# Kernel optimization log

Measured on AMD Instinct MI355X. Metric: run time of the kernel, lower is better.

Reference implementation:

```python
import jax, jax.numpy as jnp
import numpy as np

N, L, D_MODEL, N_HEADS = 2, 2048, 512, 8

def setup_inputs() -> dict:
    key = jax.random.key(0)
    x = jax.random.normal(key, (N, L, D_MODEL), dtype=jnp.float32)
    return {"input_data": x}

def reference(input_data):
    n, l, _ = input_data.shape
    h = N_HEADS
    d = D_MODEL // h  # head dim
    # Q = K = V = reshaped input (the Linear projections are unused in the original forward)
    q = input_data.reshape(n, l, h, d)
    k = q
    v = q
    scale = 1.0 / jnp.sqrt(jnp.float32(d))
    # scores: [n, h, l, s]
    scores = jnp.einsum('nlhd,nshd->nhls', q, k)
    attn_weights = jax.nn.softmax(scale * scores, axis=-1)
    # updated values: [n, l, h, d]
    updated_v = jnp.einsum('nhls,nshd->nlhd', attn_weights, v)
    out = updated_v.reshape(n, l, h * d)
    # attn returned as mean over heads: permute nhls -> nlhs, mean over h -> [n, l, s]
    attn = jnp.transpose(attn_weights, (0, 2, 1, 3)).mean(axis=-2)
    return (out, attn)
```

## Files before the change

kernel.cpp:

```cpp
#include <hip/hip_runtime.h>

#define NBATCH 2
#define SEQ    2048
#define DMODEL 512
#define NH     8
#define HDIM   64
#define SCALE  0.125f

#define K2 0.1803368801111204f

#if __has_builtin(__builtin_amdgcn_exp2f)
#define EXP2(x) __builtin_amdgcn_exp2f(x)
#else
#define EXP2(x) __expf((x) * 0.6931471805599453f)
#endif

typedef __attribute__((ext_vector_type(8))) short bf16x8;
typedef __attribute__((ext_vector_type(4))) float f32x4;

__device__ __forceinline__ unsigned short f2bf(float f) {
    union { float f; unsigned u; } v; v.f = f;
    unsigned r = v.u + 0x7FFFu + ((v.u >> 16) & 1u);
    return (unsigned short)(r >> 16);
}

__device__ __forceinline__ void pack4(unsigned short* dst, float4 v) {
    unsigned long long pk = (unsigned long long)f2bf(v.x)
        | ((unsigned long long)f2bf(v.y) << 16)
        | ((unsigned long long)f2bf(v.z) << 32)
        | ((unsigned long long)f2bf(v.w) << 48);
    __builtin_memcpy(dst, &pk, 8);
}

__device__ __forceinline__ bf16x8 pack8(float4 a, float4 b) {
    bf16x8 r;
    r[0]=(short)f2bf(a.x); r[1]=(short)f2bf(a.y); r[2]=(short)f2bf(a.z); r[3]=(short)f2bf(a.w);
    r[4]=(short)f2bf(b.x); r[5]=(short)f2bf(b.y); r[6]=(short)f2bf(b.z); r[7]=(short)f2bf(b.w);
    return r;
}

__device__ __forceinline__ void gld_lds16(const unsigned short* g, unsigned short* l) {
    __builtin_amdgcn_global_load_lds(
        (const __attribute__((address_space(1))) unsigned int*)(const void*)g,
        (__attribute__((address_space(3))) unsigned int*)(void*)l, 16, 0, 0);
}

__global__ __launch_bounds__(256) void prep_kernel(const float* __restrict__ x,
                                                   unsigned short* __restrict__ xb,
                                                   unsigned short* __restrict__ xt) {
    __shared__ unsigned short Tb[64][72];
    const int bid = blockIdx.x;
    const int n = bid >> 8, h = (bid >> 5) & 7, st = bid & 31;
    const int s0 = st * 64;
    const int t = threadIdx.x;
    {
        const int s = t >> 2, d0 = (t & 3) * 16;
        const float* xp = x + ((size_t)(n*SEQ + s0 + s))*DMODEL + h*HDIM + d0;
        #pragma unroll
        for (int i = 0; i < 4; ++i) pack4(&Tb[s][d0 + 4*i], *(const float4*)(xp + 4*i));
    }
    __syncthreads();
    {
        const int s = t >> 2, d0 = (t & 3) * 16;
        unsigned short* bp = xb + ((size_t)(n*SEQ + s0 + s))*DMODEL + h*HDIM + d0;
        *(bf16x8*)bp       = *(const bf16x8*)&Tb[s][d0];
        *(bf16x8*)(bp + 8) = *(const bf16x8*)&Tb[s][d0 + 8];
    }
    {
        const int d = t >> 2, c0 = (t & 3) * 16;
        bf16x8 v0, v1;
        #pragma unroll
        for (int j = 0; j < 8; ++j) {
            v0[j] = (short)Tb[c0 + j][d];
            v1[j] = (short)Tb[c0 + 8 + j][d];
        }
        unsigned short* tp = xt + ((size_t)((n*NH + h)*HDIM + d))*SEQ + s0 + c0;
        *(bf16x8*)tp       = v0;
        *(bf16x8*)(tp + 8) = v1;
    }
}

__global__ __launch_bounds__(256) void out_kernel4(const unsigned short* __restrict__ xb,
                                                   const unsigned short* __restrict__ xt,
                                                   float* __restrict__ out,
                                                   float* __restrict__ rho,
                                                   float* __restrict__ part,
                                                   int split) {
    __shared__ unsigned short Kb[2][64*64];
    __shared__ unsigned short Vt[2][64*64];
    __shared__ unsigned short pb[64][72];

    const int i   = blockIdx.x;
    const int cps = gridDim.x >> 3;
    const int bid = (i & 7) * cps + (i >> 3);
    int n, h, lt, ss;
    if (split) { n = bid >> 9; h = (bid >> 6) & 7; lt = (bid >> 1) & 31; ss = bid & 1; }
    else       { n = bid >> 8; h = (bid >> 5) & 7; lt = bid & 31;        ss = 0;       }
    const int l0 = lt * 64;
    const int sbase = ss << 10;
    const int nch = split ? 16 : 32;

    const int tid = threadIdx.x;
    const int wv = tid >> 6, lane = tid & 63;
    const int lr = lane & 15, lg = lane >> 4;

    const unsigned short* qp = xb + ((size_t)(n*SEQ + l0 + wv*16 + lr))*DMODEL + h*HDIM + lg*8;
    const bf16x8 a0 = *(const bf16x8*)qp;
    const bf16x8 a1 = *(const bf16x8*)(qp + 32);

    bf16x8 ones;
    #pragma unroll
    for (int j = 0; j < 8; ++j) ones[j] = (short)0x3F80;

    const int srow8  = wv*8 + (lane >> 3);
    const int schunk = lane & 7;
    const unsigned short* kbase = xb + (size_t)(n*SEQ)*DMODEL + h*HDIM;
    const unsigned short* vbase = xt + ((size_t)(n*NH + h)*HDIM)*SEQ;

    auto stage = [&](int buf, int s0) {
        #pragma unroll
        for (int it = 0; it < 2; ++it) {
            const int row = it*32 + srow8;
            const int gc  = schunk ^ (row & 7);
            gld_lds16(kbase + (size_t)(s0 + row)*DMODEL + gc*8,
                      &Kb[buf][it*2048 + wv*512]);
        }
        #pragma unroll
        for (int it = 0; it < 2; ++it) {
            const int d  = it*32 + srow8;
            const int gc = schunk ^ (d & 7);
            gld_lds16(vbase + (size_t)d*SEQ + s0 + gc*8,
                      &Vt[buf][it*2048 + wv*512]);
        }
    };

    f32x4 ov0 = {0.f,0.f,0.f,0.f}, ov1 = {0.f,0.f,0.f,0.f};
    f32x4 ov2 = {0.f,0.f,0.f,0.f}, ov3 = {0.f,0.f,0.f,0.f};
    f32x4 ovS = {0.f,0.f,0.f,0.f};

    stage(0, sbase);
    __syncthreads();
    int cur = 0;

    for (int c = 0; c < nch; ++c) {
        if (c < nch - 1) stage(cur ^ 1, sbase + (c + 1) * 64);

        const int c0 = (lg ^ (lr & 7)) << 3;
        #pragma unroll
        for (int ct = 0; ct < 4; ++ct) {
            const unsigned short* kr = &Kb[cur][(ct*16 + lr)*64];
            bf16x8 b0 = *(const bf16x8*)&kr[c0];
            bf16x8 b1 = *(const bf16x8*)&kr[c0 ^ 32];
            f32x4 acc = {0.f,0.f,0.f,0.f};
            acc = __builtin_amdgcn_mfma_f32_16x16x32_bf16(b0, a0, acc, 0,0,0);
            acc = __builtin_amdgcn_mfma_f32_16x16x32_bf16(b1, a1, acc, 0,0,0);
            const float e0 = EXP2(acc[0] * K2);
            const float e1 = EXP2(acc[1] * K2);
            const float e2 = EXP2(acc[2] * K2);
            const float e3 = EXP2(acc[3] * K2);
            unsigned long long pk = (unsigned long long)f2bf(e0)
                | ((unsigned long long)f2bf(e1) << 16)
                | ((unsigned long long)f2bf(e2) << 32)
                | ((unsigned long long)f2bf(e3) << 48);
            __builtin_memcpy(&pb[wv*16 + lr][ct*16 + lg*4], &pk, 8);
        }
        #pragma unroll
        for (int ks = 0; ks < 2; ++ks) {
            const bf16x8 pa = *(const bf16x8*)&pb[wv*16 + lr][ks*32 + lg*8];
            const int cc = ((ks*4 + lg) ^ (lr & 7)) << 3;
            const bf16x8 w0 = *(const bf16x8*)&Vt[cur][( 0 + lr)*64 + cc];
            const bf16x8 w1 = *(const bf16x8*)&Vt[cur][(16 + lr)*64 + cc];
            const bf16x8 w2 = *(const bf16x8*)&Vt[cur][(32 + lr)*64 + cc];
            const bf16x8 w3 = *(const bf16x8*)&Vt[cur][(48 + lr)*64 + cc];
            ov0 = __builtin_amdgcn_mfma_f32_16x16x32_bf16(pa, w0, ov0, 0,0,0);
            ov1 = __builtin_amdgcn_mfma_f32_16x16x32_bf16(pa, w1, ov1, 0,0,0);
            ov2 = __builtin_amdgcn_mfma_f32_16x16x32_bf16(pa, w2, ov2, 0,0,0);
            ov3 = __builtin_amdgcn_mfma_f32_16x16x32_bf16(pa, w3, ov3, 0,0,0);
            ovS = __builtin_amdgcn_mfma_f32_16x16x32_bf16(pa, ones, ovS, 0,0,0);
        }
        __syncthreads();
        cur ^= 1;
    }

    if (split) {
        float* pp = part + ((size_t)(((n*NH + h)*32 + lt)*2 + ss))*4160;
        #pragma unroll
        for (int r = 0; r < 4; ++r) {
            const int qloc = wv*16 + lg*4 + r;
            float* op = pp + qloc*64 + lr;
            op[0]  = ov0[r];
            op[16] = ov1[r];
            op[32] = ov2[r];
            op[48] = ov3[r];
        }
        if (lr == 0) {
            #pragma unroll
            for (int r = 0; r < 4; ++r)
                pp[4096 + wv*16 + lg*4 + r] = ovS[r];
        }
    } else {
        const int row0 = l0 + wv*16 + lg*4;
        if (lr == 0) {
            #pragma unroll
            for (int r = 0; r < 4; ++r)
                rho[(size_t)(n*NH + h)*SEQ + row0 + r] = ovS[r];
        }
        #pragma unroll
        for (int r = 0; r < 4; ++r) {
            const float iv = 1.f / ovS[r];
            float* op = out + ((size_t)(n*SEQ + row0 + r))*DMODEL + h*HDIM + lr;
            op[0]  = ov0[r] * iv;
            op[16] = ov1[r] * iv;
            op[32] = ov2[r] * iv;
            op[48] = ov3[r] * iv;
        }
    }
}

__global__ __launch_bounds__(256) void combine_kernel(const float* __restrict__ part,
                                                      float* __restrict__ out,
                                                      float* __restrict__ rho) {
    const int bid = blockIdx.x;
    const int n = bid >> 8, h = (bid >> 5) & 7, lt = bid & 31;
    const int l0 = lt * 64;
    const int tid = threadIdx.x;
    const int q = tid >> 2, dg = (tid & 3) * 16;

    const float* p0 = part + ((size_t)(((n*NH + h)*32 + lt)*2))*4160;
    const float* p1 = p0 + 4160;
    const float rs = p0[4096 + q] + p1[4096 + q];
    const float iv = 1.f / rs;
    if ((tid & 3) == 0)
        rho[(size_t)(n*NH + h)*SEQ + l0 + q] = rs;

    float* op = out + ((size_t)(n*SEQ + l0 + q))*DMODEL + h*HDIM + dg;
    #pragma unroll
    for (int i = 0; i < 4; ++i) {
        float4 a = *(const float4*)&p0[q*64 + dg + 4*i];
        float4 b = *(const float4*)&p1[q*64 + dg + 4*i];
        float4 o = { (a.x+b.x)*iv, (a.y+b.y)*iv, (a.z+b.z)*iv, (a.w+b.w)*iv };
        *(float4*)&op[4*i] = o;
    }
}

__global__ __launch_bounds__(256) void mean_kernel4(const unsigned short* __restrict__ xb,
                                                    const float* __restrict__ rho,
                                                    float* __restrict__ attn) {
    __shared__ unsigned short Qb[2][64*64];
    __shared__ unsigned short Kb[2][64*64];
    __shared__ float invb[NH][64];

    const int i   = blockIdx.x;
    const int bid = (i & 7) * 256 + (i >> 3);
    const int n = bid >> 10, lt = (bid >> 5) & 31, st = bid & 31;
    const int l0 = lt * 64, s0 = st * 64;
    const int tid = threadIdx.x;
    const int wv = tid >> 6, lane = tid & 63;
    const int lr = lane & 15, lg = lane >> 4;

    for (int j = tid; j < NH*64; j += 256) {
        const int hh = j >> 6, row = j & 63;
        invb[hh][row] = 0.125f / rho[(size_t)(n*NH + hh)*SEQ + l0 + row];
    }

    const int srow8  = wv*8 + (lane >> 3);
    const int schunk = lane & 7;

    auto stage = [&](int buf, int h) {
        #pragma unroll
        for (int it = 0; it < 2; ++it) {
            const int row = it*32 + srow8;
            const int gc  = schunk ^ (row & 7);
            gld_lds16(xb + ((size_t)(n*SEQ + l0 + row))*DMODEL + h*HDIM + gc*8,
                      &Qb[buf][it*2048 + wv*512]);
        }
        #pragma unroll
        for (int it = 0; it < 2; ++it) {
            const int row = it*32 + srow8;
            const int gc  = schunk ^ (row & 7);
            gld_lds16(xb + ((size_t)(n*SEQ + s0 + row))*DMODEL + h*HDIM + gc*8,
                      &Kb[buf][it*2048 + wv*512]);
        }
    };

    float mean[4][4];
    #pragma unroll
    for (int ct = 0; ct < 4; ++ct)
        #pragma unroll
        for (int r = 0; r < 4; ++r) mean[ct][r] = 0.f;

    stage(0, 0);
    __syncthreads();
    int cur = 0;

    for (int h = 0; h < NH; ++h) {
        if (h < NH-1) stage(cur ^ 1, h + 1);

        const int qrow = wv*16 + lr;
        const int c0 = (lg ^ (lr & 7)) << 3;
        const bf16x8 a0 = *(const bf16x8*)&Qb[cur][qrow*64 + c0];
        const bf16x8 a1 = *(const bf16x8*)&Qb[cur][qrow*64 + (c0 ^ 32)];
        const float logiv = __log2f(invb[h][wv*16 + lr]);
        #pragma unroll
        for (int ct = 0; ct < 4; ++ct) {
            const unsigned short* kr = &Kb[cur][(ct*16 + lr)*64];
            bf16x8 b0 = *(const bf16x8*)&kr[c0];
            bf16x8 b1 = *(const bf16x8*)&kr[c0 ^ 32];
            f32x4 acc = {0.f,0.f,0.f,0.f};
            acc = __builtin_amdgcn_mfma_f32_16x16x32_bf16(b0, a0, acc, 0,0,0);
            acc = __builtin_amdgcn_mfma_f32_16x16x32_bf16(b1, a1, acc, 0,0,0);
            #pragma unroll
            for (int r = 0; r < 4; ++r)
                mean[ct][r] += EXP2(fmaf(acc[r], K2, logiv));
        }
        __syncthreads();
        cur ^= 1;
    }

    const int arow = n*SEQ + l0 + wv*16 + lr;
    #pragma unroll
    for (int ct = 0; ct < 4; ++ct) {
        float4 v = { mean[ct][0], mean[ct][1], mean[ct][2], mean[ct][3] };
        *(float4*)&attn[(size_t)arow*SEQ + s0 + ct*16 + lg*4] = v;
    }
}

__global__ __launch_bounds__(256) void fb_out_kernel(const float* __restrict__ x,
                                                     float* __restrict__ out,
                                                     float* __restrict__ rho) {
    __shared__ unsigned short Kbuf[128][72];
    __shared__ unsigned short vT[64][136];
    __shared__ unsigned short pbuf[64][136];
    const int bid = blockIdx.x;
    const int n  = bid >> 8, h = (bid >> 5) & 7, lt = bid & 31;
    const int l0 = lt * 64;
    const int tid = threadIdx.x;
    const int wv  = tid >> 6, lane = tid & 63;
    const int lr  = lane & 15, lg = lane >> 4;
    const float* qp = x + ((size_t)(n*SEQ + l0 + wv*16 + lr))*DMODEL + h*HDIM + lg*8;
    const bf16x8 a0 = pack8(*(const float4*)qp,      *(const float4*)(qp+4));
    const bf16x8 a1 = pack8(*(const float4*)(qp+32), *(const float4*)(qp+36));
    f32x4 ov0 = {0.f,0.f,0.f,0.f}, ov1 = {0.f,0.f,0.f,0.f};
    f32x4 ov2 = {0.f,0.f,0.f,0.f}, ov3 = {0.f,0.f,0.f,0.f};
    float rs[4] = {0.f,0.f,0.f,0.f};
    for (int s0 = 0; s0 < SEQ; s0 += 128) {
        __syncthreads();
        {
            const int srow = tid >> 1, dbase = (tid & 1) * 32;
            const float* kp = x + ((size_t)(n*SEQ + s0 + srow))*DMODEL + h*HDIM + dbase;
            #pragma unroll
            for (int i = 0; i < 8; ++i) {
                float4 v = *(const float4*)(kp + 4*i);
                pack4(&Kbuf[srow][dbase + 4*i], v);
                const int d = dbase + 4*i;
                vT[d+0][srow] = f2bf(v.x); vT[d+1][srow] = f2bf(v.y);
                vT[d+2][srow] = f2bf(v.z); vT[d+3][srow] = f2bf(v.w);
            }
        }
        __syncthreads();
        #pragma unroll
        for (int ct = 0; ct < 8; ++ct) {
            const unsigned short* bp = &Kbuf[ct*16 + lr][lg*8];
            bf16x8 b0 = *(const bf16x8*)bp;
            bf16x8 b1 = *(const bf16x8*)(bp + 32);
            f32x4 acc = {0.f,0.f,0.f,0.f};
            acc = __builtin_amdgcn_mfma_f32_16x16x32_bf16(a0, b0, acc, 0,0,0);
            acc = __builtin_amdgcn_mfma_f32_16x16x32_bf16(a1, b1, acc, 0,0,0);
            #pragma unroll
            for (int r = 0; r < 4; ++r) {
                const float e = __expf(acc[r] * SCALE);
                rs[r] += e;
                pbuf[wv*16 + lg*4 + r][ct*16 + lr] = f2bf(e);
            }
        }
        __syncthreads();
        #pragma unroll
        for (int ks = 0; ks < 4; ++ks) {
            bf16x8 pa = *(const bf16x8*)&pbuf[wv*16 + lr][ks*32 + lg*8];
            bf16x8 v0 = *(const bf16x8*)&vT[ 0 + lr][ks*32 + lg*8];
            bf16x8 v1 = *(const bf16x8*)&vT[16 + lr][ks*32 + lg*8];
            bf16x8 v2 = *(const bf16x8*)&vT[32 + lr][ks*32 + lg*8];
            bf16x8 v3 = *(const bf16x8*)&vT[48 + lr][ks*32 + lg*8];
            ov0 = __builtin_amdgcn_mfma_f32_16x16x32_bf16(pa, v0, ov0, 0,0,0);
            ov1 = __builtin_amdgcn_mfma_f32_16x16x32_bf16(pa, v1, ov1, 0,0,0);
            ov2 = __builtin_amdgcn_mfma_f32_16x16x32_bf16(pa, v2, ov2, 0,0,0);
            ov3 = __builtin_amdgcn_mfma_f32_16x16x32_bf16(pa, v3, ov3, 0,0,0);
        }
    }
    #pragma unroll
    for (int r = 0; r < 4; ++r) {
        float s = rs[r];
        s += __shfl_xor(s, 1, 16); s += __shfl_xor(s, 2, 16);
        s += __shfl_xor(s, 4, 16); s += __shfl_xor(s, 8, 16);
        rs[r] = s;
    }
    const int row0 = l0 + wv*16 + lg*4;
    if (lr == 0) {
        #pragma unroll
        for (int r = 0; r < 4; ++r)
            rho[(size_t)(n*NH + h)*SEQ + row0 + r] = rs[r];
    }
    #pragma unroll
    for (int r = 0; r < 4; ++r) {
        const float iv = 1.f / rs[r];
        float* op = out + ((size_t)(n*SEQ + row0 + r))*DMODEL + h*HDIM + lr;
        op[0] = ov0[r]*iv; op[16] = ov1[r]*iv; op[32] = ov2[r]*iv; op[48] = ov3[r]*iv;
    }
}

__global__ __launch_bounds__(256) void fb_mean_kernel(const float* __restrict__ x,
                                                      const float* __restrict__ rho,
                                                      float* __restrict__ attn) {
    __shared__ unsigned short Qb[64][72];
    __shared__ unsigned short Kb[128][72];
    __shared__ float          invb[64];
    const int bid = blockIdx.x;
    const int n  = bid >> 9, lt = (bid >> 4) & 31, st = bid & 15;
    const int l0 = lt * 64, s0 = st * 128;
    const int tid = threadIdx.x;
    const int wv  = tid >> 6, lane = tid & 63;
    const int lr  = lane & 15, lg = lane >> 4;
    float mean[8][4];
    #pragma unroll
    for (int ct = 0; ct < 8; ++ct)
        #pragma unroll
        for (int r = 0; r < 4; ++r) mean[ct][r] = 0.f;
    for (int h = 0; h < NH; ++h) {
        __syncthreads();
        {
            const int qrow = tid >> 2, qd = (tid & 3) * 16;
            const float* qp = x + ((size_t)(n*SEQ + l0 + qrow))*DMODEL + h*HDIM + qd;
            #pragma unroll
            for (int i = 0; i < 4; ++i)
                pack4(&Qb[qrow][qd + 4*i], *(const float4*)(qp + 4*i));
        }
        {
            const int srow = tid >> 1, dbase = (tid & 1) * 32;
            const float* kp = x + ((size_t)(n*SEQ + s0 + srow))*DMODEL + h*HDIM + dbase;
            #pragma unroll
            for (int i = 0; i < 8; ++i)
                pack4(&Kb[srow][dbase + 4*i], *(const float4*)(kp + 4*i));
        }
        if (tid < 64)
            invb[tid] = 0.125f / rho[(size_t)(n*NH + h)*SEQ + l0 + tid];
        __syncthreads();
        const unsigned short* ap = &Qb[wv*16 + lr][lg*8];
        const bf16x8 a0 = *(const bf16x8*)ap;
        const bf16x8 a1 = *(const bf16x8*)(ap + 32);
        #pragma unroll
        for (int ct = 0; ct < 8; ++ct) {
            const unsigned short* bp = &Kb[ct*16 + lr][lg*8];
            bf16x8 b0 = *(const bf16x8*)bp;
            bf16x8 b1 = *(const bf16x8*)(bp + 32);
            f32x4 acc = {0.f,0.f,0.f,0.f};
            acc = __builtin_amdgcn_mfma_f32_16x16x32_bf16(a0, b0, acc, 0,0,0);
            acc = __builtin_amdgcn_mfma_f32_16x16x32_bf16(a1, b1, acc, 0,0,0);
            #pragma unroll
            for (int r = 0; r < 4; ++r)
                mean[ct][r] += __expf(acc[r] * SCALE) * invb[wv*16 + lg*4 + r];
        }
    }
    #pragma unroll
    for (int ct = 0; ct < 8; ++ct)
        #pragma unroll
        for (int r = 0; r < 4; ++r)
            attn[((size_t)(n*SEQ + l0 + wv*16 + lg*4 + r))*SEQ + s0 + ct*16 + lr]
                = mean[ct][r];
}

extern "C" void kernel_launch(void* const* d_in, const int* in_sizes, int n_in,
                              void* d_out, int out_size, void* d_ws, size_t ws_size,
                              hipStream_t stream) {
    (void)in_sizes; (void)n_in; (void)out_size;
    const float* x = (const float*)d_in[0];
    float* out  = (float*)d_out;
    float* attn = out + (size_t)NBATCH*SEQ*DMODEL;
    float* rho  = (float*)d_ws;

    const size_t XB_OFF   = 131072;
    const size_t XT_OFF   = XB_OFF + 4194304;
    const size_t NEED1    = XT_OFF + 4194304;
    const size_t PART_OFF = NEED1;
    const size_t NEED2    = PART_OFF + (size_t)1024*4160*4;

    if (ws_size >= NEED1) {
        unsigned short* xb = (unsigned short*)((char*)d_ws + XB_OFF);
        unsigned short* xt = (unsigned short*)((char*)d_ws + XT_OFF);
        prep_kernel <<<dim3(512),  dim3(256), 0, stream>>>(x, xb, xt);
        if (ws_size >= NEED2) {
            float* part = (float*)((char*)d_ws + PART_OFF);
            out_kernel4   <<<dim3(1024), dim3(256), 0, stream>>>(xb, xt, out, rho, part, 1);
            combine_kernel<<<dim3(512),  dim3(256), 0, stream>>>(part, out, rho);
        } else {
            out_kernel4   <<<dim3(512),  dim3(256), 0, stream>>>(xb, xt, out, rho, nullptr, 0);
        }
        mean_kernel4<<<dim3(2048), dim3(256), 0, stream>>>(xb, rho, attn);
    } else {
        fb_out_kernel <<<dim3(512),  dim3(256), 0, stream>>>(x, out, rho);
        fb_mean_kernel<<<dim3(1024), dim3(256), 0, stream>>>(x, rho, attn);
    }
}
```

Baseline: 84.69 us.

## Rewrite attention output kernel with 32x32x16 MFMA and register-resident P

```diff
diff --git a/kernel.cpp b/kernel.cpp
--- a/kernel.cpp
+++ b/kernel.cpp
@@ -15,8 +15,9 @@
 #define EXP2(x) __expf((x) * 0.6931471805599453f)
 #endif
 
-typedef __attribute__((ext_vector_type(8))) short bf16x8;
-typedef __attribute__((ext_vector_type(4))) float f32x4;
+typedef __attribute__((ext_vector_type(8)))  short bf16x8;
+typedef __attribute__((ext_vector_type(4)))  float f32x4;
+typedef __attribute__((ext_vector_type(16))) float f32x16;
 
 __device__ __forceinline__ unsigned short f2bf(float f) {
     union { float f; unsigned u; } v; v.f = f;
@@ -37,6 +38,12 @@
     r[0]=(short)f2bf(a.x); r[1]=(short)f2bf(a.y); r[2]=(short)f2bf(a.z); r[3]=(short)f2bf(a.w);
     r[4]=(short)f2bf(b.x); r[5]=(short)f2bf(b.y); r[6]=(short)f2bf(b.z); r[7]=(short)f2bf(b.w);
     return r;
+}
+
+__device__ __forceinline__ unsigned cvt_pk_bf16(float s0, float s1) {
+    unsigned d;
+    asm("v_cvt_pk_bf16_f32 %0, %1, %2" : "=v"(d) : "v"(s0), "v"(s1));
+    return d;
 }
 
 __device__ __forceinline__ void gld_lds16(const unsigned short* g, unsigned short* l) {
@@ -80,15 +87,14 @@
     }
 }
 
-__global__ __launch_bounds__(256) void out_kernel4(const unsigned short* __restrict__ xb,
-                                                   const unsigned short* __restrict__ xt,
-                                                   float* __restrict__ out,
-                                                   float* __restrict__ rho,
-                                                   float* __restrict__ part,
-                                                   int split) {
+__global__ __launch_bounds__(256, 4) void out_kernel5(const unsigned short* __restrict__ xb,
+                                                      const unsigned short* __restrict__ xt,
+                                                      float* __restrict__ out,
+                                                      float* __restrict__ rho,
+                                                      float* __restrict__ part,
+                                                      int split) {
     __shared__ unsigned short Kb[2][64*64];
     __shared__ unsigned short Vt[2][64*64];
-    __shared__ unsigned short pb[64][72];
 
     const int i   = blockIdx.x;
     const int cps = gridDim.x >> 3;
@@ -102,15 +108,15 @@
 
     const int tid = threadIdx.x;
     const int wv = tid >> 6, lane = tid & 63;
-    const int lr = lane & 15, lg = lane >> 4;
-
-    const unsigned short* qp = xb + ((size_t)(n*SEQ + l0 + wv*16 + lr))*DMODEL + h*HDIM + lg*8;
-    const bf16x8 a0 = *(const bf16x8*)qp;
-    const bf16x8 a1 = *(const bf16x8*)(qp + 32);
-
-    bf16x8 ones;
-    #pragma unroll
-    for (int j = 0; j < 8; ++j) ones[j] = (short)0x3F80;
+    const int lrow = lane & 31;
+    const int hi = lane >> 5;
+    const int qh = wv & 1, sh = wv >> 1;
+
+    const unsigned short* qg = xb + ((size_t)(n*SEQ + l0 + qh*32 + lrow))*DMODEL + h*HDIM;
+    bf16x8 qf[4];
+    #pragma unroll
+    for (int kst = 0; kst < 4; ++kst)
+        qf[kst] = *(const bf16x8*)(qg + kst*16 + hi*8);
 
     const int srow8  = wv*8 + (lane >> 3);
     const int schunk = lane & 7;
@@ -134,9 +140,10 @@
         }
     };
 
-    f32x4 ov0 = {0.f,0.f,0.f,0.f}, ov1 = {0.f,0.f,0.f,0.f};
-    f32x4 ov2 = {0.f,0.f,0.f,0.f}, ov3 = {0.f,0.f,0.f,0.f};
-    f32x4 ovS = {0.f,0.f,0.f,0.f};
+    f32x16 ovA = {0.f}, ovB = {0.f};
+    #pragma unroll
+    for (int r = 0; r < 16; ++r) { ovA[r] = 0.f; ovB[r] = 0.f; }
+    float rs = 0.f;
 
     stage(0, sbase);
     __syncthreads();
@@ -145,74 +152,90 @@
     for (int c = 0; c < nch; ++c) {
         if (c < nch - 1) stage(cur ^ 1, sbase + (c + 1) * 64);
 
-        const int c0 = (lg ^ (lr & 7)) << 3;
-        #pragma unroll
-        for (int ct = 0; ct < 4; ++ct) {
-            const unsigned short* kr = &Kb[cur][(ct*16 + lr)*64];
-            bf16x8 b0 = *(const bf16x8*)&kr[c0];
-            bf16x8 b1 = *(const bf16x8*)&kr[c0 ^ 32];
-            f32x4 acc = {0.f,0.f,0.f,0.f};
-            acc = __builtin_amdgcn_mfma_f32_16x16x32_bf16(b0, a0, acc, 0,0,0);
-            acc = __builtin_amdgcn_mfma_f32_16x16x32_bf16(b1, a1, acc, 0,0,0);
-            const float e0 = EXP2(acc[0] * K2);
-            const float e1 = EXP2(acc[1] * K2);
-            const float e2 = EXP2(acc[2] * K2);
-            const float e3 = EXP2(acc[3] * K2);
-            unsigned long long pk = (unsigned long long)f2bf(e0)
-                | ((unsigned long long)f2bf(e1) << 16)
-                | ((unsigned long long)f2bf(e2) << 32)
-                | ((unsigned long long)f2bf(e3) << 48);
-            __builtin_memcpy(&pb[wv*16 + lr][ct*16 + lg*4], &pk, 8);
-        }
-        #pragma unroll
-        for (int ks = 0; ks < 2; ++ks) {
-            const bf16x8 pa = *(const bf16x8*)&pb[wv*16 + lr][ks*32 + lg*8];
-            const int cc = ((ks*4 + lg) ^ (lr & 7)) << 3;
-            const bf16x8 w0 = *(const bf16x8*)&Vt[cur][( 0 + lr)*64 + cc];
-            const bf16x8 w1 = *(const bf16x8*)&Vt[cur][(16 + lr)*64 + cc];
-            const bf16x8 w2 = *(const bf16x8*)&Vt[cur][(32 + lr)*64 + cc];
-            const bf16x8 w3 = *(const bf16x8*)&Vt[cur][(48 + lr)*64 + cc];
-            ov0 = __builtin_amdgcn_mfma_f32_16x16x32_bf16(pa, w0, ov0, 0,0,0);
-            ov1 = __builtin_amdgcn_mfma_f32_16x16x32_bf16(pa, w1, ov1, 0,0,0);
-            ov2 = __builtin_amdgcn_mfma_f32_16x16x32_bf16(pa, w2, ov2, 0,0,0);
-            ov3 = __builtin_amdgcn_mfma_f32_16x16x32_bf16(pa, w3, ov3, 0,0,0);
-            ovS = __builtin_amdgcn_mfma_f32_16x16x32_bf16(pa, ones, ovS, 0,0,0);
+        f32x16 acc;
+        #pragma unroll
+        for (int r = 0; r < 16; ++r) acc[r] = 0.f;
+        #pragma unroll
+        for (int kst = 0; kst < 4; ++kst) {
+            const int g = ((kst*2 + hi) ^ (lrow & 7)) << 3;
+            const bf16x8 kf = *(const bf16x8*)&Kb[cur][(sh*32 + lrow)*64 + g];
+            acc = __builtin_amdgcn_mfma_f32_32x32x16_bf16(kf, qf[kst], acc, 0, 0, 0);
+        }
+        #pragma unroll
+        for (int r = 0; r < 16; ++r) {
+            acc[r] = EXP2(acc[r] * K2);
+            rs += acc[r];
+        }
+        #pragma unroll
+        for (int p = 0; p < 2; ++p) {
+            const unsigned g0 = cvt_pk_bf16(acc[8*p+0], acc[8*p+1]);
+            const unsigned g1 = cvt_pk_bf16(acc[8*p+2], acc[8*p+3]);
+            const unsigned g2 = cvt_pk_bf16(acc[8*p+4], acc[8*p+5]);
+            const unsigned g3 = cvt_pk_bf16(acc[8*p+6], acc[8*p+7]);
+            const unsigned b0 = hi ? g0 : g2;
+            const unsigned b1 = hi ? g1 : g3;
+            const unsigned r0 = (unsigned)__shfl_xor((int)b0, 32);
+            const unsigned r1 = (unsigned)__shfl_xor((int)b1, 32);
+            union { unsigned u[4]; bf16x8 h8; } pf;
+            pf.u[0] = hi ? r0 : g0;
+            pf.u[1] = hi ? r1 : g1;
+            pf.u[2] = hi ? g2 : r0;
+            pf.u[3] = hi ? g3 : r1;
+            const int gv = ((sh*4 + p*2 + hi) ^ (lrow & 7)) << 3;
+            const bf16x8 v0 = *(const bf16x8*)&Vt[cur][( 0 + lrow)*64 + gv];
+            const bf16x8 v1 = *(const bf16x8*)&Vt[cur][(32 + lrow)*64 + gv];
+            ovA = __builtin_amdgcn_mfma_f32_32x32x16_bf16(v0, pf.h8, ovA, 0, 0, 0);
+            ovB = __builtin_amdgcn_mfma_f32_32x32x16_bf16(v1, pf.h8, ovB, 0, 0, 0);
         }
         __syncthreads();
         cur ^= 1;
     }
 
-    if (split) {
-        float* pp = part + ((size_t)(((n*NH + h)*32 + lt)*2 + ss))*4160;
-        #pragma unroll
-        for (int r = 0; r < 4; ++r) {
-            const int qloc = wv*16 + lg*4 + r;
-            float* op = pp + qloc*64 + lr;
-            op[0]  = ov0[r];
-            op[16] = ov1[r];
-            op[32] = ov2[r];
-            op[48] = ov3[r];
-        }
-        if (lr == 0) {
-            #pragma unroll
-            for (int r = 0; r < 4; ++r)
-                pp[4096 + wv*16 + lg*4 + r] = ovS[r];
-        }
-    } else {
-        const int row0 = l0 + wv*16 + lg*4;
-        if (lr == 0) {
-            #pragma unroll
-            for (int r = 0; r < 4; ++r)
-                rho[(size_t)(n*NH + h)*SEQ + row0 + r] = ovS[r];
-        }
-        #pragma unroll
-        for (int r = 0; r < 4; ++r) {
-            const float iv = 1.f / ovS[r];
-            float* op = out + ((size_t)(n*SEQ + row0 + r))*DMODEL + h*HDIM + lr;
-            op[0]  = ov0[r] * iv;
-            op[16] = ov1[r] * iv;
-            op[32] = ov2[r] * iv;
-            op[48] = ov3[r] * iv;
+    rs += __shfl_xor(rs, 32);
+    float* red = (float*)&Vt[0][0];
+    float* rsr = (float*)&Kb[0][0];
+    if (sh == 1) {
+        #pragma unroll
+        for (int g = 0; g < 4; ++g) {
+            float4 a = { ovA[4*g+0], ovA[4*g+1], ovA[4*g+2], ovA[4*g+3] };
+            float4 b = { ovB[4*g+0], ovB[4*g+1], ovB[4*g+2], ovB[4*g+3] };
+            *(float4*)&red[qh*2048 + lrow*64 +  0 + g*8 + 4*hi] = a;
+            *(float4*)&red[qh*2048 + lrow*64 + 32 + g*8 + 4*hi] = b;
+        }
+        if (hi == 0) rsr[qh*32 + lrow] = rs;
+    }
+    __syncthreads();
+    if (sh == 0) {
+        const float rs_tot = rs + rsr[qh*32 + lrow];
+        #pragma unroll
+        for (int g = 0; g < 4; ++g) {
+            float4 a = *(const float4*)&red[qh*2048 + lrow*64 +  0 + g*8 + 4*hi];
+            float4 b = *(const float4*)&red[qh*2048 + lrow*64 + 32 + g*8 + 4*hi];
+            ovA[4*g+0]+=a.x; ovA[4*g+1]+=a.y; ovA[4*g+2]+=a.z; ovA[4*g+3]+=a.w;
+            ovB[4*g+0]+=b.x; ovB[4*g+1]+=b.y; ovB[4*g+2]+=b.z; ovB[4*g+3]+=b.w;
+        }
+        const int qloc = qh*32 + lrow;
+        if (split) {
+            float* pp = part + ((size_t)(((n*NH + h)*32 + lt)*2 + ss))*4160;
+            #pragma unroll
+            for (int g = 0; g < 4; ++g) {
+                float4 a = { ovA[4*g+0], ovA[4*g+1], ovA[4*g+2], ovA[4*g+3] };
+                float4 b = { ovB[4*g+0], ovB[4*g+1], ovB[4*g+2], ovB[4*g+3] };
+                *(float4*)&pp[qloc*64 +  0 + g*8 + 4*hi] = a;
+                *(float4*)&pp[qloc*64 + 32 + g*8 + 4*hi] = b;
+            }
+            if (hi == 0) pp[4096 + qloc] = rs_tot;
+        } else {
+            const float iv = 1.f / rs_tot;
+            float* op = out + ((size_t)(n*SEQ + l0 + qloc))*DMODEL + h*HDIM;
+            #pragma unroll
+            for (int g = 0; g < 4; ++g) {
+                float4 a = { ovA[4*g+0]*iv, ovA[4*g+1]*iv, ovA[4*g+2]*iv, ovA[4*g+3]*iv };
+                float4 b = { ovB[4*g+0]*iv, ovB[4*g+1]*iv, ovB[4*g+2]*iv, ovB[4*g+3]*iv };
+                *(float4*)&op[ 0 + g*8 + 4*hi] = a;
+                *(float4*)&op[32 + g*8 + 4*hi] = b;
+            }
+            if (hi == 0) rho[(size_t)(n*NH + h)*SEQ + l0 + qloc] = rs_tot;
         }
     }
 }
@@ -489,10 +512,10 @@
         prep_kernel <<<dim3(512),  dim3(256), 0, stream>>>(x, xb, xt);
         if (ws_size >= NEED2) {
             float* part = (float*)((char*)d_ws + PART_OFF);
-            out_kernel4   <<<dim3(1024), dim3(256), 0, stream>>>(xb, xt, out, rho, part, 1);
+            out_kernel5   <<<dim3(1024), dim3(256), 0, stream>>>(xb, xt, out, rho, part, 1);
             combine_kernel<<<dim3(512),  dim3(256), 0, stream>>>(part, out, rho);
         } else {
-            out_kernel4   <<<dim3(512),  dim3(256), 0, stream>>>(xb, xt, out, rho, nullptr, 0);
+            out_kernel5   <<<dim3(512),  dim3(256), 0, stream>>>(xb, xt, out, rho, nullptr, 0);
         }
         mean_kernel4<<<dim3(2048), dim3(256), 0, stream>>>(xb, rho, attn);
     } else {
```

After: 77.60 us. -8.4%, faster.
